# Kernel tuning notes

Hardware: AMD Instinct MI355X
Metric: run time of the kernel (lower is better)

The kernel has to match this reference:

```python
import jax, jax.numpy as jnp
import numpy as np

B, S, F, H = 2, 2048, 1024, 16
D = F // H  # 64 head dim


def setup_inputs() -> dict:
    key = jax.random.key(0)
    ks = jax.random.split(key, 11)
    std = 1.0 / np.sqrt(F)
    inp = {
        "q": jax.random.normal(ks[0], (B, S, F), dtype=jnp.float32),
        "k": jax.random.normal(ks[1], (B, S, F), dtype=jnp.float32),
        "v": jax.random.normal(ks[2], (B, S, F), dtype=jnp.float32),
        "wq_w": jax.random.normal(ks[3], (F, F), dtype=jnp.float32) * std,
        "wq_b": jnp.zeros((F,), dtype=jnp.float32),
        "wk_w": jax.random.normal(ks[4], (F, F), dtype=jnp.float32) * std,
        "wk_b": jnp.zeros((F,), dtype=jnp.float32),
        "wv_w": jax.random.normal(ks[5], (F, F), dtype=jnp.float32) * std,
        "wv_b": jnp.zeros((F,), dtype=jnp.float32),
        "fc_w": jax.random.normal(ks[6], (F, F), dtype=jnp.float32) * std,
        "fc_b": jnp.zeros((F,), dtype=jnp.float32),
    }
    return inp


def _split_heads(x):
    # [B, S, F] -> [B, H, S, D]
    return x.reshape(B, S, H, D).transpose(0, 2, 1, 3)


def reference(q, k, v, wq_w, wq_b, wk_w, wk_b, wv_w, wv_b, fc_w, fc_b):
    # Linear projections (torch Linear: x @ W^T + b)
    qh = _split_heads(q @ wq_w.T + wq_b)
    kh = _split_heads(k @ wk_w.T + wk_b)
    vh = _split_heads(v @ wv_w.T + wv_b)
    # scaled dot product attention, explicit [B,H,S,S] scores as in source
    scale = 1.0 / np.sqrt(D)
    scores = jnp.einsum("bhqd,bhkd->bhqk", qh, kh) * scale
    attn = jax.nn.softmax(scores, axis=-1)
    ctx = jnp.einsum("bhqk,bhkd->bhqd", attn, vh)
    # merge heads: [B,H,S,D] -> [B,S,F]
    concat = ctx.transpose(0, 2, 1, 3).reshape(B, S, F)
    out = concat @ fc_w.T + fc_b
    out = jax.nn.relu(out)  # activation=F.relu_ default
    return (out, attn)
```

## Files before the change

### kernel.cpp

```cpp
#include <hip/hip_runtime.h>
#include <stdint.h>

#define DEV __device__ __forceinline__

using f32x4  = __attribute__((ext_vector_type(4))) float;
using bf16x8 = __attribute__((ext_vector_type(8))) __bf16;
using bf16x4 = __attribute__((ext_vector_type(4))) __bf16;

static constexpr int SEQ  = 2048;
static constexpr int FEA  = 1024;
static constexpr int NHEAD = 16;
static constexpr int MROWS = 4096;
static constexpr float QK_SCALE = 0.18033688011112042f;

DEV f32x4 mfma16(bf16x8 a, bf16x8 b, f32x4 c) {
  return __builtin_amdgcn_mfma_f32_16x16x32_bf16(a, b, c, 0, 0, 0);
}

DEV void gload16(const void* g, void* l) {
  __builtin_amdgcn_global_load_lds((__attribute__((address_space(1))) void*)g,
                                   (__attribute__((address_space(3))) void*)l,
                                   16, 0, 0);
}

#define FENCE_VMCNT(n) asm volatile("s_waitcnt vmcnt(" #n ")" ::: "memory")
#define FENCE_LGKM0()  asm volatile("s_waitcnt lgkmcnt(0)" ::: "memory")

struct ConvSeg { const float* src; __bf16* dst; int n4; float scale; };
struct ConvArgs { ConvSeg seg[7]; };

__global__ __launch_bounds__(256) void convert_k(ConvArgs a) {
  const ConvSeg sg = a.seg[blockIdx.y];
  const int stride = gridDim.x * blockDim.x;
  for (int i = blockIdx.x * blockDim.x + threadIdx.x; i < sg.n4; i += stride) {
    const f32x4 v = *(const f32x4*)(sg.src + (size_t)i * 4);
    bf16x4 o = {(__bf16)(v[0] * sg.scale), (__bf16)(v[1] * sg.scale),
                (__bf16)(v[2] * sg.scale), (__bf16)(v[3] * sg.scale)};
    *(bf16x4*)(sg.dst + (size_t)i * 4) = o;
  }
}

DEV void gemm_core64(const __bf16* __restrict__ A, const __bf16* __restrict__ Bt,
                     char* lds, int row0, int col0, int tid, f32x4 (&acc)[4][4]) {
  char* Alds = lds;
  char* Blds = lds + 16384;
  constexpr int K = 1024;
  const int lane = tid & 63;
  const int w    = tid >> 6;
  const int ci   = lane & 15;
  const int g    = lane >> 4;
  const int wr   = w >> 1, wc = w & 1;

  const __bf16* gA[4]; const __bf16* gB[4];
  char* lA[4]; char* lB[4];
#pragma unroll
  for (int j = 0; j < 4; ++j) {
    const int c = tid + 256 * j;
    const int r = c >> 3, s = c & 7;
    const int gsw = (s ^ (r & 7)) * 8;
    gA[j] = A  + (size_t)(row0 + r) * K + gsw;
    gB[j] = Bt + (size_t)(col0 + r) * K + gsw;
    lA[j] = Alds + c * 16;
    lB[j] = Blds + c * 16;
  }
  const int rsw = (ci & 7) << 4;

  for (int k0 = 0; k0 < K; k0 += 64) {
    __syncthreads();
#pragma unroll
    for (int j = 0; j < 4; ++j) {
      gload16(gA[j] + k0, lA[j]);
      gload16(gB[j] + k0, lB[j]);
    }
    __syncthreads();
#pragma unroll
    for (int kk = 0; kk < 2; ++kk) {
      bf16x8 af[4], bfr[4];
#pragma unroll
      for (int m = 0; m < 4; ++m)
        af[m] = *(const bf16x8*)(Alds + (wr * 64 + m * 16 + ci) * 128 +
                                 ((kk * 64 + g * 16) ^ rsw));
#pragma unroll
      for (int n = 0; n < 4; ++n)
        bfr[n] = *(const bf16x8*)(Blds + (wc * 64 + n * 16 + ci) * 128 +
                                  ((kk * 64 + g * 16) ^ rsw));
#pragma unroll
      for (int m = 0; m < 4; ++m)
#pragma unroll
        for (int n = 0; n < 4; ++n)
          acc[m][n] = mfma16(af[m], bfr[n], acc[m][n]);
    }
  }
}

struct QkvArgs {
  const __bf16* A[3];
  const __bf16* Bt[3];
  const float*  bias[3];
  float         bscale[3];
  __bf16*       out[3];
};

__global__ __launch_bounds__(256) void gemm_qkv(QkvArgs args) {
  __shared__ __align__(16) char lds[32768];
  const int z = blockIdx.z;
  const int tid = threadIdx.x;
  const int row0 = blockIdx.x * 128;
  const int col0 = blockIdx.y * 128;
  f32x4 acc[4][4] = {};
  gemm_core64(args.A[z], args.Bt[z], lds, row0, col0, tid, acc);

  const int lane = tid & 63;
  const int ci = lane & 15, g = lane >> 4;
  const int w = tid >> 6;
  const int wr = w >> 1, wc = w & 1;
  const float* bias = args.bias[z];
  const float bscale = args.bscale[z];
  __bf16* outp = args.out[z];
  const bool vt = (z == 2);
#pragma unroll
  for (int m = 0; m < 4; ++m)
#pragma unroll
    for (int n = 0; n < 4; ++n)
#pragma unroll
      for (int r = 0; r < 4; ++r) {
        const int gr = row0 + wr * 64 + m * 16 + 4 * g + r;
        const int gc = col0 + wc * 64 + n * 16 + ci;
        const float vv = acc[m][n][r] + bias[gc] * bscale;
        const int b = gr >> 11, s = gr & (SEQ - 1);
        const int h = gc >> 6,  d = gc & 63;
        if (!vt)
          outp[(((size_t)b * NHEAD + h) * SEQ + s) * 64 + d] = (__bf16)vv;
        else
          outp[(((size_t)b * NHEAD + h) * 64 + d) * SEQ + s] = (__bf16)vv;
      }
}

__global__ __launch_bounds__(256) void gemm_fc(const __bf16* __restrict__ A,
                                               const __bf16* __restrict__ Bt,
                                               const float* __restrict__ bias,
                                               float* __restrict__ outp) {
  __shared__ __align__(16) char lds[32768];
  const int tid = threadIdx.x;
  const int row0 = blockIdx.x * 128;
  const int col0 = blockIdx.y * 128;
  f32x4 acc[4][4] = {};
  gemm_core64(A, Bt, lds, row0, col0, tid, acc);

  const int lane = tid & 63;
  const int ci = lane & 15, g = lane >> 4;
  const int w = tid >> 6;
  const int wr = w >> 1, wc = w & 1;
#pragma unroll
  for (int m = 0; m < 4; ++m)
#pragma unroll
    for (int n = 0; n < 4; ++n)
#pragma unroll
      for (int r = 0; r < 4; ++r) {
        const int gr = row0 + wr * 64 + m * 16 + 4 * g + r;
        const int gc = col0 + wc * 64 + n * 16 + ci;
        const float vv = fmaxf(acc[m][n][r] + bias[gc], 0.0f);
        __builtin_nontemporal_store(vv, &outp[(size_t)gr * FEA + gc]);
      }
}

static constexpr int QBLK = 32;
static constexpr int KVB  = 128;
static constexpr int NT   = SEQ / KVB;

__global__ __launch_bounds__(512, 4) void attn_fused(const __bf16* __restrict__ Qh,
                                                     const __bf16* __restrict__ Kh,
                                                     const __bf16* __restrict__ VhT,
                                                     float* __restrict__ attn_out,
                                                     __bf16* __restrict__ Cbuf) {
  __shared__ __align__(16) char smem[65536];
  __shared__ float rs_lds[8][16];
  __shared__ float linv_lds[QBLK];
  float* pvf = (float*)smem;

  const int tid  = threadIdx.x;
  const int lane = tid & 63;
  const int w    = tid >> 6;
  const int ci   = lane & 15;
  const int g    = lane >> 4;
  const int qg   = w >> 2;
  const int kg   = w & 3;

  const int id   = blockIdx.x;
  const int xcd  = id & 7;
  const int idx  = id >> 3;
  const int bh   = xcd * 4 + (idx >> 6);
  const int qblk = idx & 63;

  const __bf16* Qp   = Qh + ((size_t)bh * SEQ + qblk * QBLK) * 64;
  const char*   Kbyt = (const char*)(Kh  + (size_t)bh * SEQ * 64);
  const char*   Vbyt = (const char*)(VhT + (size_t)bh * 64 * SEQ);

  const int cA = tid, cB = tid + 512;
  const int kgoffA = ((cA >> 3) * 128) + (((cA & 7) ^ ((cA >> 3) & 7)) * 16);
  const int kgoffB = ((cB >> 3) * 128) + (((cB & 7) ^ ((cB >> 3) & 7)) * 16);
  const int vdA = cA >> 4, vdB = cB >> 4;
  const int vgoffA = vdA * (SEQ * 2) + (((cA & 15) ^ (vdA & 7)) * 16);
  const int vgoffB = vdB * (SEQ * 2) + (((cB & 15) ^ (vdB & 7)) * 16);

#define STAGE_K(t, boff) { gload16(Kbyt + (size_t)(t) * 16384 + kgoffA, smem + (boff) + cA * 16); \
                           gload16(Kbyt + (size_t)(t) * 16384 + kgoffB, smem + (boff) + cB * 16); }
#define STAGE_V(t, boff) { gload16(Vbyt + (size_t)(t) * 256 + vgoffA, smem + 16384 + (boff) + cA * 16); \
                           gload16(Vbyt + (size_t)(t) * 256 + vgoffB, smem + 16384 + (boff) + cB * 16); }

  const bf16x8 q0 = *(const bf16x8*)(Qp + (qg * 16 + ci) * 64 + 8 * g);
  const bf16x8 q1 = *(const bf16x8*)(Qp + (qg * 16 + ci) * 64 + 32 + 8 * g);

  const int kswz  = (ci & 7) << 4;
  const int krow0 = kg * 4096 + ci * 128;

  float rs = 0.f;
  STAGE_K(0, 0);
  for (int t = 0; t < NT; ++t) {
    const int coff = (t & 1) << 15;
    if (t < NT - 1) { STAGE_K(t + 1, coff ^ 32768); FENCE_VMCNT(2); }
    else            { FENCE_VMCNT(0); }
    __builtin_amdgcn_s_barrier();
    const char* kt = smem + coff + krow0;
#pragma unroll
    for (int s = 0; s < 2; ++s) {
      const bf16x8 k0 = *(const bf16x8*)(kt + s * 2048 + ((16 * g) ^ kswz));
      const bf16x8 k1 = *(const bf16x8*)(kt + s * 2048 + ((64 + 16 * g) ^ kswz));
      f32x4 sf = {0.f, 0.f, 0.f, 0.f};
      sf = mfma16(k0, q0, sf);
      sf = mfma16(k1, q1, sf);
#pragma unroll
      for (int r = 0; r < 4; ++r) rs += __builtin_amdgcn_exp2f(sf[r]);
    }
    FENCE_LGKM0();
    __builtin_amdgcn_s_barrier();
  }
  rs += __shfl_xor(rs, 16);
  rs += __shfl_xor(rs, 32);
  if (lane < 16) rs_lds[w][lane] = rs;
  __syncthreads();
  if (tid < QBLK) {
    const int qg2 = tid >> 4;
    float tsum = 0.f;
#pragma unroll
    for (int kk = 0; kk < 4; ++kk) tsum += rs_lds[qg2 * 4 + kk][tid & 15];
    linv_lds[tid] = -__log2f(tsum);
  }
  __syncthreads();
  const float linv = linv_lds[qg * 16 + ci];

  f32x4 apv[4] = {};
  float* orow = attn_out + ((size_t)bh * SEQ + qblk * QBLK + qg * 16 + ci) * SEQ +
                kg * 32 + 4 * g;

  STAGE_K(0, 0);
  STAGE_V(0, 0);
  for (int t = 0; t < NT; ++t) {
    const int coff = (t & 1) << 15;
    if (t < NT - 1) { STAGE_K(t + 1, coff ^ 32768); STAGE_V(t + 1, coff ^ 32768); FENCE_VMCNT(4); }
    else            { FENCE_VMCNT(0); }
    __builtin_amdgcn_s_barrier();

    f32x4 e[2];
#pragma unroll
    for (int s = 0; s < 2; ++s) {
      const char* kt = smem + coff + krow0 + s * 2048;
      const bf16x8 k0 = *(const bf16x8*)(kt + ((16 * g) ^ kswz));
      const bf16x8 k1 = *(const bf16x8*)(kt + ((64 + 16 * g) ^ kswz));
      f32x4 sf = {0.f, 0.f, 0.f, 0.f};
      sf = mfma16(k0, q0, sf);
      sf = mfma16(k1, q1, sf);
#pragma unroll
      for (int r = 0; r < 4; ++r) e[s][r] = __builtin_amdgcn_exp2f(sf[r] + linv);
      __builtin_nontemporal_store(e[s], (f32x4*)(orow + t * 128 + s * 16));
    }
    const bf16x8 pa = {(__bf16)e[0][0], (__bf16)e[0][1], (__bf16)e[0][2], (__bf16)e[0][3],
                       (__bf16)e[1][0], (__bf16)e[1][1], (__bf16)e[1][2], (__bf16)e[1][3]};
    const int inr0 = (64 * kg + 8 * g) ^ kswz;
    const int inr1 = (64 * kg + 32 + 8 * g) ^ kswz;
#pragma unroll
    for (int dt = 0; dt < 4; ++dt) {
      const char* vrow = smem + 16384 + coff + (dt * 16 + ci) * 256;
      const bf16x4 v0 = *(const bf16x4*)(vrow + inr0);
      const bf16x4 v1 = *(const bf16x4*)(vrow + inr1);
      const bf16x8 vb = {v0[0], v0[1], v0[2], v0[3], v1[0], v1[1], v1[2], v1[3]};
      apv[dt] = mfma16(pa, vb, apv[dt]);
    }
    FENCE_LGKM0();
    __builtin_amdgcn_s_barrier();
  }

  {
    const int base = (qg * 4 + kg) * 16;
#pragma unroll
    for (int dt = 0; dt < 4; ++dt)
#pragma unroll
      for (int r = 0; r < 4; ++r)
        pvf[(base + 4 * g + r) * 68 + dt * 16 + ci] = apv[dt][r];
  }
  __syncthreads();
  {
    const int qq  = tid >> 4;
    const int d0  = (tid & 15) * 4;
    const int qg2 = qq >> 4, row = qq & 15;
    f32x4 s = {0.f, 0.f, 0.f, 0.f};
#pragma unroll
    for (int kk = 0; kk < 4; ++kk)
      s += *(const f32x4*)&pvf[((qg2 * 4 + kk) * 16 + row) * 68 + d0];
    const int b = bh >> 4, h = bh & 15;
    const bf16x4 o = {(__bf16)s[0], (__bf16)s[1], (__bf16)s[2], (__bf16)s[3]};
    *(bf16x4*)&Cbuf[((size_t)b * SEQ + qblk * QBLK + qq) * FEA + h * 64 + d0] = o;
  }
#undef STAGE_K
#undef STAGE_V
}

extern "C" void kernel_launch(void* const* d_in, const int* in_sizes, int n_in,
                              void* d_out, int out_size, void* d_ws, size_t ws_size,
                              hipStream_t stream) {
  const float* q    = (const float*)d_in[0];
  const float* k    = (const float*)d_in[1];
  const float* v    = (const float*)d_in[2];
  const float* wq_w = (const float*)d_in[3];
  const float* wq_b = (const float*)d_in[4];
  const float* wk_w = (const float*)d_in[5];
  const float* wk_b = (const float*)d_in[6];
  const float* wv_w = (const float*)d_in[7];
  const float* wv_b = (const float*)d_in[8];
  const float* fc_w = (const float*)d_in[9];
  const float* fc_b = (const float*)d_in[10];

  float* out0 = (float*)d_out;
  float* attn = out0 + (size_t)MROWS * FEA;

  __bf16* Xq = (__bf16*)attn;
  __bf16* Xk = Xq + (size_t)MROWS * FEA;
  __bf16* Xv = Xk + (size_t)MROWS * FEA;
  __bf16* Wq = Xv + (size_t)MROWS * FEA;
  __bf16* Wk = Wq + (size_t)FEA * FEA;
  __bf16* Wv = Wk + (size_t)FEA * FEA;

  __bf16* Qh  = (__bf16*)d_ws;
  __bf16* Kh  = Qh  + (size_t)MROWS * FEA;
  __bf16* VhT = Kh  + (size_t)MROWS * FEA;
  __bf16* Cb  = VhT + (size_t)MROWS * FEA;
  __bf16* Wfc = Cb  + (size_t)MROWS * FEA;

  ConvArgs ca;
  ca.seg[0] = {q,    Xq,  (MROWS * FEA) / 4, 1.0f};
  ca.seg[1] = {k,    Xk,  (MROWS * FEA) / 4, 1.0f};
  ca.seg[2] = {v,    Xv,  (MROWS * FEA) / 4, 1.0f};
  ca.seg[3] = {wq_w, Wq,  (FEA * FEA) / 4,   QK_SCALE};
  ca.seg[4] = {wk_w, Wk,  (FEA * FEA) / 4,   1.0f};
  ca.seg[5] = {wv_w, Wv,  (FEA * FEA) / 4,   1.0f};
  ca.seg[6] = {fc_w, Wfc, (FEA * FEA) / 4,   1.0f};
  convert_k<<<dim3(512, 7), 256, 0, stream>>>(ca);

  QkvArgs qa;
  qa.A[0] = Xq; qa.Bt[0] = Wq; qa.bias[0] = wq_b; qa.bscale[0] = QK_SCALE; qa.out[0] = Qh;
  qa.A[1] = Xk; qa.Bt[1] = Wk; qa.bias[1] = wk_b; qa.bscale[1] = 1.0f;     qa.out[1] = Kh;
  qa.A[2] = Xv; qa.Bt[2] = Wv; qa.bias[2] = wv_b; qa.bscale[2] = 1.0f;     qa.out[2] = VhT;
  gemm_qkv<<<dim3(MROWS / 128, FEA / 128, 3), 256, 0, stream>>>(qa);

  attn_fused<<<dim3((SEQ / QBLK) * NHEAD * 2), 512, 0, stream>>>(Qh, Kh, VhT, attn, Cb);

  gemm_fc<<<dim3(MROWS / 128, FEA / 128), 256, 0, stream>>>(Cb, Wfc, fc_b, out0);
}
```

Baseline: 236.1 us.

## Process two 16-row query tiles per warp in fused attention kernel

Doubles the query block per workgroup from 32 to 64 rows. Each warp now computes two 16-row query tiles against the same K and V fragments read from LDS, which halves the K/V staging traffic and LDS reads per query row. The softmax row sums, normalisation, stores and context reduction are extended to match, and the vmcnt fence counts are adjusted for the extra stores. In exchange it uses more registers and launches half as many workgroups, which may reduce occupancy and latency hiding while the kernel is dominated by the large attn_out writes.

```diff
diff --git a/kernel.cpp b/kernel.cpp
--- a/kernel.cpp
+++ b/kernel.cpp
@@ -164,7 +164,7 @@
       }
 }
 
-static constexpr int QBLK = 32;
+static constexpr int QBLK = 64;
 static constexpr int KVB  = 128;
 static constexpr int NT   = SEQ / KVB;
 
@@ -174,7 +174,7 @@
                                                      float* __restrict__ attn_out,
                                                      __bf16* __restrict__ Cbuf) {
   __shared__ __align__(16) char smem[65536];
-  __shared__ float rs_lds[8][16];
+  __shared__ float rs_lds[8][32];
   __shared__ float linv_lds[QBLK];
   float* pvf = (float*)smem;
 
@@ -189,8 +189,8 @@
   const int id   = blockIdx.x;
   const int xcd  = id & 7;
   const int idx  = id >> 3;
-  const int bh   = xcd * 4 + (idx >> 6);
-  const int qblk = idx & 63;
+  const int bh   = xcd * 4 + (idx >> 5);
+  const int qblk = idx & 31;
 
   const __bf16* Qp   = Qh + ((size_t)bh * SEQ + qblk * QBLK) * 64;
   const char*   Kbyt = (const char*)(Kh  + (size_t)bh * SEQ * 64);
@@ -208,13 +208,17 @@
 #define STAGE_V(t, boff) { gload16(Vbyt + (size_t)(t) * 256 + vgoffA, smem + 16384 + (boff) + cA * 16); \
                            gload16(Vbyt + (size_t)(t) * 256 + vgoffB, smem + 16384 + (boff) + cB * 16); }
 
-  const bf16x8 q0 = *(const bf16x8*)(Qp + (qg * 16 + ci) * 64 + 8 * g);
-  const bf16x8 q1 = *(const bf16x8*)(Qp + (qg * 16 + ci) * 64 + 32 + 8 * g);
+  bf16x8 qa0[2], qa1[2];
+#pragma unroll
+  for (int u = 0; u < 2; ++u) {
+    qa0[u] = *(const bf16x8*)(Qp + (qg * 32 + u * 16 + ci) * 64 + 8 * g);
+    qa1[u] = *(const bf16x8*)(Qp + (qg * 32 + u * 16 + ci) * 64 + 32 + 8 * g);
+  }
 
   const int kswz  = (ci & 7) << 4;
   const int krow0 = kg * 4096 + ci * 128;
 
-  float rs = 0.f;
+  float rs0 = 0.f, rs1 = 0.f;
   STAGE_K(0, 0);
   for (int t = 0; t < NT; ++t) {
     const int coff = (t & 1) << 15;
@@ -226,56 +230,79 @@
     for (int s = 0; s < 2; ++s) {
       const bf16x8 k0 = *(const bf16x8*)(kt + s * 2048 + ((16 * g) ^ kswz));
       const bf16x8 k1 = *(const bf16x8*)(kt + s * 2048 + ((64 + 16 * g) ^ kswz));
-      f32x4 sf = {0.f, 0.f, 0.f, 0.f};
-      sf = mfma16(k0, q0, sf);
-      sf = mfma16(k1, q1, sf);
-#pragma unroll
-      for (int r = 0; r < 4; ++r) rs += __builtin_amdgcn_exp2f(sf[r]);
+      f32x4 sa = {0.f, 0.f, 0.f, 0.f}, sb = {0.f, 0.f, 0.f, 0.f};
+      sa = mfma16(k0, qa0[0], sa);
+      sa = mfma16(k1, qa1[0], sa);
+      sb = mfma16(k0, qa0[1], sb);
+      sb = mfma16(k1, qa1[1], sb);
+#pragma unroll
+      for (int r = 0; r < 4; ++r) {
+        rs0 += __builtin_amdgcn_exp2f(sa[r]);
+        rs1 += __builtin_amdgcn_exp2f(sb[r]);
+      }
     }
     FENCE_LGKM0();
     __builtin_amdgcn_s_barrier();
   }
-  rs += __shfl_xor(rs, 16);
-  rs += __shfl_xor(rs, 32);
-  if (lane < 16) rs_lds[w][lane] = rs;
+  rs0 += __shfl_xor(rs0, 16); rs0 += __shfl_xor(rs0, 32);
+  rs1 += __shfl_xor(rs1, 16); rs1 += __shfl_xor(rs1, 32);
+  if (lane < 16) { rs_lds[w][lane] = rs0; rs_lds[w][16 + lane] = rs1; }
   __syncthreads();
   if (tid < QBLK) {
-    const int qg2 = tid >> 4;
+    const int qg2 = tid >> 5, ur = tid & 31;
     float tsum = 0.f;
 #pragma unroll
-    for (int kk = 0; kk < 4; ++kk) tsum += rs_lds[qg2 * 4 + kk][tid & 15];
+    for (int kk = 0; kk < 4; ++kk) tsum += rs_lds[qg2 * 4 + kk][ur];
     linv_lds[tid] = -__log2f(tsum);
   }
   __syncthreads();
-  const float linv = linv_lds[qg * 16 + ci];
-
-  f32x4 apv[4] = {};
-  float* orow = attn_out + ((size_t)bh * SEQ + qblk * QBLK + qg * 16 + ci) * SEQ +
-                kg * 32 + 4 * g;
+  const float linv0 = linv_lds[qg * 32 + ci];
+  const float linv1 = linv_lds[qg * 32 + 16 + ci];
+
+  f32x4 apv[2][4] = {};
+  float* orow0 = attn_out + ((size_t)bh * SEQ + qblk * QBLK + qg * 32 + ci) * SEQ +
+                 kg * 32 + 4 * g;
+  float* orow1 = orow0 + (size_t)16 * SEQ;
 
   STAGE_K(0, 0);
   STAGE_V(0, 0);
+  FENCE_VMCNT(0);
+  __syncthreads();
   for (int t = 0; t < NT; ++t) {
     const int coff = (t & 1) << 15;
-    if (t < NT - 1) { STAGE_K(t + 1, coff ^ 32768); STAGE_V(t + 1, coff ^ 32768); FENCE_VMCNT(4); }
-    else            { FENCE_VMCNT(0); }
+    if (t < NT - 1) { STAGE_K(t + 1, coff ^ 32768); STAGE_V(t + 1, coff ^ 32768); FENCE_VMCNT(8); }
+    else            { FENCE_VMCNT(4); }
     __builtin_amdgcn_s_barrier();
 
-    f32x4 e[2];
+    f32x4 sf0[2], sf1[2];
 #pragma unroll
     for (int s = 0; s < 2; ++s) {
       const char* kt = smem + coff + krow0 + s * 2048;
       const bf16x8 k0 = *(const bf16x8*)(kt + ((16 * g) ^ kswz));
       const bf16x8 k1 = *(const bf16x8*)(kt + ((64 + 16 * g) ^ kswz));
-      f32x4 sf = {0.f, 0.f, 0.f, 0.f};
-      sf = mfma16(k0, q0, sf);
-      sf = mfma16(k1, q1, sf);
-#pragma unroll
-      for (int r = 0; r < 4; ++r) e[s][r] = __builtin_amdgcn_exp2f(sf[r] + linv);
-      __builtin_nontemporal_store(e[s], (f32x4*)(orow + t * 128 + s * 16));
-    }
-    const bf16x8 pa = {(__bf16)e[0][0], (__bf16)e[0][1], (__bf16)e[0][2], (__bf16)e[0][3],
-                       (__bf16)e[1][0], (__bf16)e[1][1], (__bf16)e[1][2], (__bf16)e[1][3]};
+      f32x4 sa = {0.f, 0.f, 0.f, 0.f}, sb = {0.f, 0.f, 0.f, 0.f};
+      sa = mfma16(k0, qa0[0], sa);
+      sa = mfma16(k1, qa1[0], sa);
+      sb = mfma16(k0, qa0[1], sb);
+      sb = mfma16(k1, qa1[1], sb);
+      sf0[s] = sa; sf1[s] = sb;
+    }
+    f32x4 e00, e01, e10, e11;
+#pragma unroll
+    for (int r = 0; r < 4; ++r) {
+      e00[r] = __builtin_amdgcn_exp2f(sf0[0][r] + linv0);
+      e01[r] = __builtin_amdgcn_exp2f(sf0[1][r] + linv0);
+      e10[r] = __builtin_amdgcn_exp2f(sf1[0][r] + linv1);
+      e11[r] = __builtin_amdgcn_exp2f(sf1[1][r] + linv1);
+    }
+    __builtin_nontemporal_store(e00, (f32x4*)(orow0 + t * 128));
+    __builtin_nontemporal_store(e01, (f32x4*)(orow0 + t * 128 + 16));
+    __builtin_nontemporal_store(e10, (f32x4*)(orow1 + t * 128));
+    __builtin_nontemporal_store(e11, (f32x4*)(orow1 + t * 128 + 16));
+    const bf16x8 pa0 = {(__bf16)e00[0], (__bf16)e00[1], (__bf16)e00[2], (__bf16)e00[3],
+                        (__bf16)e01[0], (__bf16)e01[1], (__bf16)e01[2], (__bf16)e01[3]};
+    const bf16x8 pa1 = {(__bf16)e10[0], (__bf16)e10[1], (__bf16)e10[2], (__bf16)e10[3],
+                        (__bf16)e11[0], (__bf16)e11[1], (__bf16)e11[2], (__bf16)e11[3]};
     const int inr0 = (64 * kg + 8 * g) ^ kswz;
     const int inr1 = (64 * kg + 32 + 8 * g) ^ kswz;
 #pragma unroll
@@ -284,32 +311,34 @@
       const bf16x4 v0 = *(const bf16x4*)(vrow + inr0);
       const bf16x4 v1 = *(const bf16x4*)(vrow + inr1);
       const bf16x8 vb = {v0[0], v0[1], v0[2], v0[3], v1[0], v1[1], v1[2], v1[3]};
-      apv[dt] = mfma16(pa, vb, apv[dt]);
+      apv[0][dt] = mfma16(pa0, vb, apv[0][dt]);
+      apv[1][dt] = mfma16(pa1, vb, apv[1][dt]);
     }
     FENCE_LGKM0();
     __builtin_amdgcn_s_barrier();
   }
 
-  {
+  const int b = bh >> 4, h = bh & 15;
+#pragma unroll
+  for (int u = 0; u < 2; ++u) {
+    __syncthreads();
     const int base = (qg * 4 + kg) * 16;
 #pragma unroll
     for (int dt = 0; dt < 4; ++dt)
 #pragma unroll
       for (int r = 0; r < 4; ++r)
-        pvf[(base + 4 * g + r) * 68 + dt * 16 + ci] = apv[dt][r];
-  }
-  __syncthreads();
-  {
+        pvf[(base + 4 * g + r) * 68 + dt * 16 + ci] = apv[u][dt][r];
+    __syncthreads();
     const int qq  = tid >> 4;
     const int d0  = (tid & 15) * 4;
     const int qg2 = qq >> 4, row = qq & 15;
-    f32x4 s = {0.f, 0.f, 0.f, 0.f};
+    f32x4 ss = {0.f, 0.f, 0.f, 0.f};
 #pragma unroll
     for (int kk = 0; kk < 4; ++kk)
-      s += *(const f32x4*)&pvf[((qg2 * 4 + kk) * 16 + row) * 68 + d0];
-    const int b = bh >> 4, h = bh & 15;
-    const bf16x4 o = {(__bf16)s[0], (__bf16)s[1], (__bf16)s[2], (__bf16)s[3]};
-    *(bf16x4*)&Cbuf[((size_t)b * SEQ + qblk * QBLK + qq) * FEA + h * 64 + d0] = o;
+      ss += *(const f32x4*)&pvf[((qg2 * 4 + kk) * 16 + row) * 68 + d0];
+    const int srow = qblk * QBLK + qg2 * 32 + u * 16 + row;
+    const bf16x4 o = {(__bf16)ss[0], (__bf16)ss[1], (__bf16)ss[2], (__bf16)ss[3]};
+    *(bf16x4*)&Cbuf[((size_t)b * SEQ + srow) * FEA + h * 64 + d0] = o;
   }
 #undef STAGE_K
 #undef STAGE_V
```

Result: slower. 250.0 us (+5.9%).
